# Performance work log

Hardware: AMD Instinct MI355X
Metric: run time of the kernel (lower is better)

The kernel has to match this reference:

```python
import jax, jax.numpy as jnp
import numpy as np

HIDDEN = 2048
NUM_HEADS = 16
HEAD_DIM = 128
INNER = NUM_HEADS * HEAD_DIM
ROPE_BASE = 10000.0


def apply_rope(x):
    # x: [B, H, S, D], rotate-half (NeoX-style) RoPE
    B, H, S, D = x.shape
    inv_freq = 1.0 / (ROPE_BASE ** (jnp.arange(0, D, 2, dtype=jnp.float32) / D))
    t = jnp.arange(S, dtype=jnp.float32)
    freqs = t[:, None] * inv_freq[None, :]          # [S, D/2]
    cos = jnp.concatenate([jnp.cos(freqs)] * 2, -1)  # [S, D]
    sin = jnp.concatenate([jnp.sin(freqs)] * 2, -1)
    x1, x2 = x[..., : D // 2], x[..., D // 2:]
    rotated = jnp.concatenate([-x2, x1], axis=-1)
    return x * cos[None, None] + rotated * sin[None, None]


def setup_inputs() -> dict:
    key = jax.random.key(0)
    ks = jax.random.split(key, 9)
    s = 1.0 / np.sqrt(HIDDEN)
    return {
        "hidden_states": jax.random.normal(ks[0], (2, 2048, HIDDEN), jnp.float32),
        "Wq": jax.random.uniform(ks[1], (INNER, HIDDEN), jnp.float32, -s, s),
        "bq": jax.random.uniform(ks[2], (INNER,), jnp.float32, -s, s),
        "Wk": jax.random.uniform(ks[3], (INNER, HIDDEN), jnp.float32, -s, s),
        "bk": jax.random.uniform(ks[4], (INNER,), jnp.float32, -s, s),
        "Wv": jax.random.uniform(ks[5], (INNER, HIDDEN), jnp.float32, -s, s),
        "bv": jax.random.uniform(ks[6], (INNER,), jnp.float32, -s, s),
        "Wo": jax.random.uniform(ks[7], (HIDDEN, INNER), jnp.float32, -s, s),
        "bo": jax.random.uniform(ks[8], (HIDDEN,), jnp.float32, -s, s),
    }


def reference(hidden_states, Wq, bq, Wk, bk, Wv, bv, Wo, bo):
    B, S, _ = hidden_states.shape

    def heads(x):  # [B,S,inner] -> [B,H,S,D]
        return x.reshape(B, S, NUM_HEADS, HEAD_DIM).transpose(0, 2, 1, 3)

    q = heads(hidden_states @ Wq.T + bq)
    k = heads(hidden_states @ Wk.T + bk)
    v = heads(hidden_states @ Wv.T + bv)
    q = apply_rope(q)
    k = apply_rope(k)

    scores = jnp.einsum("bhqd,bhkd->bhqk", q, k) / jnp.sqrt(
        jnp.asarray(HEAD_DIM, q.dtype))
    causal = jnp.tril(jnp.ones((S, S), dtype=bool))
    scores = jnp.where(causal[None, None], scores, jnp.finfo(scores.dtype).min)
    weights = jax.nn.softmax(scores, axis=-1)
    context = jnp.einsum("bhqk,bhkd->bhqd", weights, v)
    merged = context.transpose(0, 2, 1, 3).reshape(B, S, INNER)
    return merged @ Wo.T + bo
```

## Files before the change

### kernel.cpp

```cpp
#include <hip/hip_runtime.h>

using u16 = unsigned short;
using u32 = unsigned int;

typedef __attribute__((ext_vector_type(4))) float f32x4;
typedef __attribute__((ext_vector_type(8))) short frag8;

#define HIDDEN 2048
#define SEQ    2048
#define NHEADS 16
#define HDIM   128

__device__ __forceinline__ float bf2f(u16 u) {
  union { u32 i; float f; } c; c.i = ((u32)u) << 16; return c.f;
}
__device__ __forceinline__ u16 f2bf(float f) {
  union { float f; u32 i; } c; c.f = f;
  u32 u = c.i + 0x7fffu + ((c.i >> 16) & 1u);
  return (u16)(u >> 16);
}

__global__ void cvt_all(const float* __restrict__ X,
                        const float* __restrict__ W0, const float* __restrict__ W1,
                        const float* __restrict__ W2, const float* __restrict__ W3,
                        u16* __restrict__ dX,
                        u16* __restrict__ dW0, u16* __restrict__ dW1,
                        u16* __restrict__ dW2, u16* __restrict__ dW3)
{
  const int bx = blockIdx.x;
  const float* s; u16* d; int g;
  if (bx < 4096) { s = X; d = dX; g = bx * 256 + threadIdx.x; }
  else {
    const int t = bx - 4096;
    const int w = t >> 11;
    s = (w == 0) ? W0 : (w == 1) ? W1 : (w == 2) ? W2 : W3;
    d = (w == 0) ? dW0 : (w == 1) ? dW1 : (w == 2) ? dW2 : dW3;
    g = (t & 2047) * 256 + threadIdx.x;
  }
  const float* p = s + (size_t)g * 8;
  f32x4 x0 = *(const f32x4*)p, x1 = *(const f32x4*)(p + 4);
  frag8 o;
#pragma unroll
  for (int e = 0; e < 4; e++) { o[e] = (short)f2bf(x0[e]); o[e+4] = (short)f2bf(x1[e]); }
  *(frag8*)(d + (size_t)g * 8) = o;
}

template<int W_BF16, int NW, int VT, int C_F32>
__global__ __launch_bounds__(256, 4)
void gemm_fused(const u16* __restrict__ A,
                const void* __restrict__ W0, const void* __restrict__ W1,
                const void* __restrict__ W2,
                const float* __restrict__ bias0, const float* __restrict__ bias1,
                const float* __restrict__ bias2,
                void* __restrict__ C0, void* __restrict__ C1, void* __restrict__ C2)
{
  __shared__ __align__(16) u16 smem[8192];
  u16* As = smem;
  u16* Bs = smem + 4096;

  const int tid  = threadIdx.x;
  const int lane = tid & 63;
  const int wv   = tid >> 6;
  const int quad = lane >> 4;
  const int l16  = lane & 15;
  const int wm = wv >> 1, wn = wv & 1;
  const int m0 = blockIdx.y * 128;
  const int wix = (NW == 1) ? 0 : (blockIdx.x >> 4);
  const int n0  = ((NW == 1) ? blockIdx.x : (blockIdx.x & 15)) * 128;

  const void* Wp = (wix == 0) ? W0 : (wix == 1) ? W1 : W2;
  const float* bias = (wix == 0) ? bias0 : (wix == 1) ? bias1 : bias2;
  void* Cp = (wix == 0) ? C0 : (wix == 1) ? C1 : C2;

  f32x4 acc[4][4];
#pragma unroll
  for (int i = 0; i < 4; i++)
#pragma unroll
    for (int j = 0; j < 4; j++) acc[i][j] = (f32x4)0.0f;

  const int g0 = tid, g1 = tid + 256;
  const int r0 = g0 >> 2, c0 = (g0 & 3) * 8;
  const int r1 = g1 >> 2, c1 = (g1 & 3) * 8;

  for (int k0 = 0; k0 < HIDDEN; k0 += 32) {
    __builtin_amdgcn_global_load_lds(
      (const __attribute__((address_space(1))) void*)(A + (size_t)(m0 + r0) * HIDDEN + k0 + c0),
      (__attribute__((address_space(3))) void*)(As + g0 * 8), 16, 0, 0);
    __builtin_amdgcn_global_load_lds(
      (const __attribute__((address_space(1))) void*)(A + (size_t)(m0 + r1) * HIDDEN + k0 + c1),
      (__attribute__((address_space(3))) void*)(As + g1 * 8), 16, 0, 0);
    if (W_BF16) {
      const u16* Wb = (const u16*)Wp;
      __builtin_amdgcn_global_load_lds(
        (const __attribute__((address_space(1))) void*)(Wb + (size_t)(n0 + r0) * HIDDEN + k0 + c0),
        (__attribute__((address_space(3))) void*)(Bs + g0 * 8), 16, 0, 0);
      __builtin_amdgcn_global_load_lds(
        (const __attribute__((address_space(1))) void*)(Wb + (size_t)(n0 + r1) * HIDDEN + k0 + c1),
        (__attribute__((address_space(3))) void*)(Bs + g1 * 8), 16, 0, 0);
    } else {
      const float* Wf = (const float*)Wp;
      const float* p0 = Wf + (size_t)(n0 + r0) * HIDDEN + k0 + c0;
      const float* p1 = Wf + (size_t)(n0 + r1) * HIDDEN + k0 + c1;
      f32x4 x0 = *(const f32x4*)p0, x1 = *(const f32x4*)(p0 + 4);
      f32x4 y0 = *(const f32x4*)p1, y1 = *(const f32x4*)(p1 + 4);
      frag8 b0v, b1v;
#pragma unroll
      for (int e = 0; e < 4; e++) {
        b0v[e]   = (short)f2bf(x0[e]); b0v[e+4] = (short)f2bf(x1[e]);
        b1v[e]   = (short)f2bf(y0[e]); b1v[e+4] = (short)f2bf(y1[e]);
      }
      *(frag8*)&Bs[g0 * 8] = b0v;
      *(frag8*)&Bs[g1 * 8] = b1v;
    }

    __builtin_amdgcn_s_waitcnt(0);
    __syncthreads();

    frag8 af[4], bfr[4];
#pragma unroll
    for (int mt = 0; mt < 4; mt++)
      af[mt] = *(const frag8*)&As[(wm*64 + mt*16 + l16) * 32 + quad*8];
#pragma unroll
    for (int nt = 0; nt < 4; nt++)
      bfr[nt] = *(const frag8*)&Bs[(wn*64 + nt*16 + l16) * 32 + quad*8];
#pragma unroll
    for (int mt = 0; mt < 4; mt++)
#pragma unroll
      for (int nt = 0; nt < 4; nt++)
        acc[mt][nt] = __builtin_amdgcn_mfma_f32_16x16x32_bf16(af[mt], bfr[nt], acc[mt][nt], 0, 0, 0);

    __syncthreads();
  }

  if (VT && wix == 2) {
    u16* Cv = (u16*)Cp;
    u16* T = smem + wv * 1056;
#pragma unroll
    for (int nt = 0; nt < 4; nt++) {
      const int n  = n0 + wn*64 + nt*16 + l16;
      const float bv = bias[n];
#pragma unroll
      for (int mt = 0; mt < 4; mt++)
#pragma unroll
        for (int r = 0; r < 4; r++)
          T[l16 * 66 + mt*16 + quad*4 + r] = f2bf(acc[mt][nt][r] + bv);
#pragma unroll
      for (int rr = 0; rr < 16; rr++) {
        const int nn = n0 + wn*64 + nt*16 + rr;
        const int mm = m0 + wm*64 + lane;
        const int b = mm >> 11, s = mm & 2047;
        Cv[((size_t)(b * HIDDEN + nn)) * SEQ + s] = T[rr * 66 + lane];
      }
    }
  } else {
#pragma unroll
    for (int nt = 0; nt < 4; nt++) {
      const int n  = n0 + wn*64 + nt*16 + l16;
      const float bv = bias[n];
#pragma unroll
      for (int mt = 0; mt < 4; mt++) {
#pragma unroll
        for (int r = 0; r < 4; r++) {
          const int m = m0 + wm*64 + mt*16 + quad*4 + r;
          if (C_F32) ((float*)Cp)[(size_t)m * HIDDEN + n] = acc[mt][nt][r] + bv;
          else       ((u16*)Cp)[(size_t)m * HIDDEN + n]   = f2bf(acc[mt][nt][r] + bv);
        }
      }
    }
  }
}

#define NT32 32

#define STG(gptr, lofs) __builtin_amdgcn_global_load_lds( \
    (const __attribute__((address_space(1))) void*)(gptr), \
    (__attribute__((address_space(3))) void*)(smem + (lofs)), 16, 0, 0)

#define GRP(t, DOSTAGE, WAITSTR) { \
  u16* As = smem + ((t) % 3) * 24576; \
  u16* Bs = As + 16384; \
  frag8 af[8], bfr[2]; \
  _Pragma("unroll") for (int mt = 0; mt < 8; mt++) \
    af[mt] = *(const frag8*)(As + abase + mt*1024 + s0q); \
  bfr[0] = *(const frag8*)(Bs + bbase + s0q); \
  bfr[1] = *(const frag8*)(Bs + bbase + 1024 + s0q); \
  if (DOSTAGE) { \
    const size_t ko = (size_t)((t)+2)*64; const int sb = (((t)+2)%3)*24576; \
    STG(gA0 + ko, sb + ldsA0); STG(gA1 + ko, sb + ldsA1); STG(gB0 + ko, sb + ldsB0); \
  } \
  __builtin_amdgcn_s_barrier(); \
  __builtin_amdgcn_s_setprio(1); \
  _Pragma("unroll") for (int mt = 0; mt < 8; mt++) { \
    acc[mt][0] = __builtin_amdgcn_mfma_f32_16x16x32_bf16(af[mt], bfr[0], acc[mt][0], 0,0,0); \
    acc[mt][1] = __builtin_amdgcn_mfma_f32_16x16x32_bf16(af[mt], bfr[1], acc[mt][1], 0,0,0); \
  } \
  __builtin_amdgcn_s_setprio(0); \
  __builtin_amdgcn_s_barrier(); \
  _Pragma("unroll") for (int mt = 0; mt < 8; mt++) \
    af[mt] = *(const frag8*)(As + abase + mt*1024 + s1q); \
  bfr[0] = *(const frag8*)(Bs + bbase + s1q); \
  bfr[1] = *(const frag8*)(Bs + bbase + 1024 + s1q); \
  if (DOSTAGE) { \
    const size_t ko = (size_t)((t)+2)*64; const int sb = (((t)+2)%3)*24576; \
    STG(gA2 + ko, sb + ldsA2); STG(gA3 + ko, sb + ldsA3); STG(gB1 + ko, sb + ldsB1); \
  } \
  __builtin_amdgcn_s_barrier(); \
  __builtin_amdgcn_s_setprio(1); \
  _Pragma("unroll") for (int mt = 0; mt < 8; mt++) { \
    acc[mt][0] = __builtin_amdgcn_mfma_f32_16x16x32_bf16(af[mt], bfr[0], acc[mt][0], 0,0,0); \
    acc[mt][1] = __builtin_amdgcn_mfma_f32_16x16x32_bf16(af[mt], bfr[1], acc[mt][1], 0,0,0); \
  } \
  __builtin_amdgcn_s_setprio(0); \
  asm volatile("s_waitcnt " WAITSTR ::: "memory"); \
  __builtin_amdgcn_s_barrier(); \
}

#define G256_SETUP(Abase, Wbase) \
  const int tid  = threadIdx.x; \
  const int lane = tid & 63; \
  const int wv   = tid >> 6; \
  const int quad = lane >> 4; \
  const int l16  = lane & 15; \
  const int wm = wv >> 2, wn = wv & 3; \
  const int c8 = (lane & 7) ^ (lane >> 3); \
  const int rA = lane >> 3; \
  const u16* gA0 = (Abase) + (size_t)(m0 + wv*32 +  0 + rA) * HIDDEN + c8*8; \
  const u16* gA1 = (Abase) + (size_t)(m0 + wv*32 +  8 + rA) * HIDDEN + c8*8; \
  const u16* gA2 = (Abase) + (size_t)(m0 + wv*32 + 16 + rA) * HIDDEN + c8*8; \
  const u16* gA3 = (Abase) + (size_t)(m0 + wv*32 + 24 + rA) * HIDDEN + c8*8; \
  const u16* gB0 = (Wbase) + (size_t)(n0 + wv*16 +  0 + rA) * HIDDEN + c8*8; \
  const u16* gB1 = (Wbase) + (size_t)(n0 + wv*16 +  8 + rA) * HIDDEN + c8*8; \
  const int ldsA0 = (4*wv)*512 + lane*8; \
  const int ldsA1 = ldsA0 + 512; \
  const int ldsA2 = ldsA0 + 1024; \
  const int ldsA3 = ldsA0 + 1536; \
  const int ldsB0 = 16384 + (2*wv)*512 + lane*8; \
  const int ldsB1 = ldsB0 + 512; \
  const int s0q = ((quad    ) ^ (l16 & 7)) * 8; \
  const int s1q = ((quad + 4) ^ (l16 & 7)) * 8; \
  const int abase = (wm*128 + l16) * 64; \
  const int bbase = (wn*32  + l16) * 64; \
  f32x4 acc[8][2]; \
  _Pragma("unroll") \
  for (int i = 0; i < 8; i++) { acc[i][0] = (f32x4)0.0f; acc[i][1] = (f32x4)0.0f; } \
  STG(gA0, ldsA0); STG(gA1, ldsA1); STG(gB0, ldsB0); \
  STG(gA2, ldsA2); STG(gA3, ldsA3); STG(gB1, ldsB1); \
  STG(gA0 + 64, 24576 + ldsA0); STG(gA1 + 64, 24576 + ldsA1); STG(gB0 + 64, 24576 + ldsB0); \
  STG(gA2 + 64, 24576 + ldsA2); STG(gA3 + 64, 24576 + ldsA3); STG(gB1 + 64, 24576 + ldsB1); \
  asm volatile("s_waitcnt vmcnt(6)" ::: "memory"); \
  __builtin_amdgcn_s_barrier(); \
  for (int t = 0; t < NT32 - 2; ++t) GRP(t, 1, "vmcnt(6)"); \
  GRP(NT32 - 2, 0, "vmcnt(0)"); \
  GRP(NT32 - 1, 0, "vmcnt(63)");

__global__ __launch_bounds__(512, 2)
void gemm256_qkv(const u16* __restrict__ A,
                 const u16* __restrict__ W0, const u16* __restrict__ W1,
                 const u16* __restrict__ W2,
                 const float* __restrict__ bias0, const float* __restrict__ bias1,
                 const float* __restrict__ bias2,
                 u16* __restrict__ C0, u16* __restrict__ C1, u16* __restrict__ Vt)
{
  __shared__ __align__(16) u16 smem[73728];

  const int bid = blockIdx.x;
  const int sbid = (bid & 7) * 96 + (bid >> 3);
  const int colTile = sbid >> 4;
  const int rowTile = sbid & 15;
  const int wix = colTile >> 4;
  const int n0  = (colTile & 15) * 128;
  const int m0  = rowTile * 256;

  const u16* Wp = (wix == 0) ? W0 : (wix == 1) ? W1 : W2;
  const float* bias = (wix == 0) ? bias0 : (wix == 1) ? bias1 : bias2;

  G256_SETUP(A, Wp)

  if (wix != 2) {
    u16* Cb = (wix == 0) ? C0 : C1;
#pragma unroll
    for (int nt = 0; nt < 2; nt++) {
      const int n = n0 + wn*32 + nt*16 + l16;
      const float bv = bias[n];
#pragma unroll
      for (int mt = 0; mt < 8; mt++) {
        const int m = m0 + wm*128 + mt*16 + quad*4;
#pragma unroll
        for (int r = 0; r < 4; r++)
          Cb[(size_t)(m + r) * HIDDEN + n] = f2bf(acc[mt][nt][r] + bv);
      }
    }
  } else {
    u16* T = smem + wv * 2176;
    const int b  = m0 >> 11;
    const int s0 = (m0 & 2047) + wm*128;
#pragma unroll
    for (int nt = 0; nt < 2; nt++) {
      const int nloc = n0 + wn*32 + nt*16;
      const float bv = bias[nloc + l16];
#pragma unroll
      for (int mt = 0; mt < 8; mt++)
#pragma unroll
        for (int r = 0; r < 4; r++)
          T[l16*136 + mt*16 + quad*4 + r] = f2bf(acc[mt][nt][r] + bv);
#pragma unroll
      for (int rr = 0; rr < 16; rr++) {
        const size_t vb = ((size_t)(b * HIDDEN + nloc + rr)) * SEQ + s0;
        Vt[vb + lane]      = T[rr*136 + lane];
        Vt[vb + 64 + lane] = T[rr*136 + 64 + lane];
      }
    }
  }
}

__global__ __launch_bounds__(512, 2)
void gemm256_o(const u16* __restrict__ A, const u16* __restrict__ W,
               const float* __restrict__ bias, float* __restrict__ C)
{
  __shared__ __align__(16) u16 smem[73728];

  const int bid = blockIdx.x;
  const int sbid = (bid & 7) * 32 + (bid >> 3);
  const int colTile = sbid >> 4;
  const int rowTile = sbid & 15;
  const int n0  = colTile * 128;
  const int m0  = rowTile * 256;

  G256_SETUP(A, W)

#pragma unroll
  for (int nt = 0; nt < 2; nt++) {
    const int n = n0 + wn*32 + nt*16 + l16;
    const float bv = bias[n];
#pragma unroll
    for (int mt = 0; mt < 8; mt++) {
      const int m = m0 + wm*128 + mt*16 + quad*4;
#pragma unroll
      for (int r = 0; r < 4; r++)
        C[(size_t)(m + r) * HIDDEN + n] = acc[mt][nt][r] + bv;
    }
  }
}

__global__ void rope_kernel(u16* __restrict__ Q, u16* __restrict__ K)
{
  const int tid = blockIdx.x * 256 + threadIdx.x;
  const int t   = tid >> 19;
  const int r   = tid & 524287;
  const int row = r >> 7;
  const int grp = r & 127;
  const int h   = grp >> 3, d0 = (grp & 7) * 8;
  u16* X = t ? K : Q;
  const float s = (float)(row & 2047);
  const float qscale = t ? 1.0f : 0.08838834764831845f;
  const size_t base = (size_t)row * HIDDEN + h * HDIM + d0;
  frag8 a = *(const frag8*)(X + base);
  frag8 b = *(const frag8*)(X + base + 64);
  frag8 oa, ob;
#pragma unroll
  for (int e = 0; e < 8; e++) {
    const float inv = __expf(-(float)(d0 + e) * (9.210340371976184f / 64.0f));
    float sn, c;
    __sincosf(s * inv, &sn, &c);
    const float x1 = bf2f((u16)a[e]), x2 = bf2f((u16)b[e]);
    oa[e] = (short)f2bf((x1 * c - x2 * sn) * qscale);
    ob[e] = (short)f2bf((x2 * c + x1 * sn) * qscale);
  }
  *(frag8*)(X + base)      = oa;
  *(frag8*)(X + base + 64) = ob;
}

#define KS_STR 132
#define VS_STR 68
#define PS_STR 68
__global__ __launch_bounds__(256, 3)
void attn_kernel(const u16* Q, const u16* __restrict__ K,
                 const u16* __restrict__ Vt, u16* O)
{
  __shared__ __align__(16) u16 Ks[64 * KS_STR];
  __shared__ __align__(16) u16 Vs[128 * VS_STR];
  __shared__ __align__(16) u16 Ps[4 * 16 * PS_STR];

  const int bx = blockIdx.x;
  const int g  = bx >> 5;
  const int bh = bx & 31;
  const int qt = (g & 1) ? (31 - (g >> 1)) : (g >> 1);
  const int b = bh >> 4, h = bh & 15;

  const int tid = threadIdx.x, lane = tid & 63, wv = tid >> 6;
  const int quad = lane >> 4, l16 = lane & 15;

  frag8 qf[4];
  const size_t qbase = ((size_t)(b * SEQ) + qt*64 + wv*16) * HIDDEN + h * HDIM;
#pragma unroll
  for (int ks = 0; ks < 4; ks++)
    qf[ks] = *(const frag8*)(Q + qbase + (size_t)l16 * HIDDEN + ks*32 + quad*8);

  f32x4 Oacc[8];
#pragma unroll
  for (int dt = 0; dt < 8; dt++) Oacc[dt] = (f32x4)0.0f;
  float m_i[4], l_i[4];
#pragma unroll
  for (int r = 0; r < 4; r++) { m_i[r] = -1e30f; l_i[r] = 0.0f; }

  const int ktmax = qt + 1;
  const size_t krow0 = (size_t)(b * SEQ) * HIDDEN + h * HDIM;
  const size_t vrow0 = (size_t)(b * HIDDEN + h * HDIM) * SEQ;
  u16* Pw = Ps + wv * (16 * PS_STR);
  const int qmin = qt*64 + wv*16;

  const int kkey = tid >> 4, kgd = (tid & 15) * 8;
  const int vd = tid >> 3, vj8 = (tid & 7) * 8;

  frag8 kreg[4], vreg[4];
#pragma unroll
  for (int it = 0; it < 4; it++) {
    kreg[it] = *(const frag8*)(K + krow0 + (size_t)(it*16 + kkey) * HIDDEN + kgd);
    vreg[it] = *(const frag8*)(Vt + vrow0 + (size_t)(it*32 + vd) * SEQ + vj8);
  }

  for (int kt = 0; kt < ktmax; kt++) {
#pragma unroll
    for (int it = 0; it < 4; it++) {
      *(frag8*)&Ks[(it*16 + kkey) * KS_STR + kgd] = kreg[it];
      *(frag8*)&Vs[(it*32 + vd) * VS_STR + vj8]  = vreg[it];
    }
    __syncthreads();

    if (kt + 1 < ktmax) {
#pragma unroll
      for (int it = 0; it < 4; it++) {
        kreg[it] = *(const frag8*)(K + krow0 + (size_t)((kt+1)*64 + it*16 + kkey) * HIDDEN + kgd);
        vreg[it] = *(const frag8*)(Vt + vrow0 + (size_t)(it*32 + vd) * SEQ + (kt+1)*64 + vj8);
      }
    }

    f32x4 st[4];
#pragma unroll
    for (int jt = 0; jt < 4; jt++) st[jt] = (f32x4)0.0f;

    __builtin_amdgcn_s_setprio(1);
#pragma unroll
    for (int ks = 0; ks < 4; ks++) {
      frag8 kf[4];
#pragma unroll
      for (int jt = 0; jt < 4; jt++)
        kf[jt] = *(const frag8*)&Ks[(jt*16 + l16) * KS_STR + ks*32 + quad*8];
#pragma unroll
      for (int jt = 0; jt < 4; jt++)
        st[jt] = __builtin_amdgcn_mfma_f32_16x16x32_bf16(qf[ks], kf[jt], st[jt], 0, 0, 0);
    }
    __builtin_amdgcn_s_setprio(0);

    if (kt == qt) {
#pragma unroll
      for (int jt = 0; jt < 4; jt++) {
        const int jl = jt*16 + l16;
#pragma unroll
        for (int r = 0; r < 4; r++) {
          const int ml = wv*16 + quad*4 + r;
          st[jt][r] = (jl <= ml) ? st[jt][r] : -1e30f;
        }
      }
    }

    float alpha[4];
    int needresc = 0;
#pragma unroll
    for (int r = 0; r < 4; r++) {
      float cm = st[0][r];
#pragma unroll
      for (int jt = 1; jt < 4; jt++) cm = fmaxf(cm, st[jt][r]);
      cm = fmaxf(cm, __shfl_xor(cm, 1, 64));
      cm = fmaxf(cm, __shfl_xor(cm, 2, 64));
      cm = fmaxf(cm, __shfl_xor(cm, 4, 64));
      cm = fmaxf(cm, __shfl_xor(cm, 8, 64));
      if (cm > m_i[r] + 8.0f) {
        alpha[r] = __expf(m_i[r] - cm);
        m_i[r] = cm;
        needresc = 1;
      } else {
        alpha[r] = 1.0f;
      }
    }

    float csum[4];
#pragma unroll
    for (int r = 0; r < 4; r++) csum[r] = 0.0f;
#pragma unroll
    for (int jt = 0; jt < 4; jt++)
#pragma unroll
      for (int r = 0; r < 4; r++) {
        const float p = __expf(st[jt][r] - m_i[r]);
        csum[r] += p;
        Pw[(quad*4 + r) * PS_STR + jt*16 + l16] = f2bf(p);
      }
#pragma unroll
    for (int r = 0; r < 4; r++) {
      float cs = csum[r];
      cs += __shfl_xor(cs, 1, 64);
      cs += __shfl_xor(cs, 2, 64);
      cs += __shfl_xor(cs, 4, 64);
      cs += __shfl_xor(cs, 8, 64);
      l_i[r] = l_i[r] * alpha[r] + cs;
    }
    if (__any(needresc)) {
#pragma unroll
      for (int r = 0; r < 4; r++)
#pragma unroll
        for (int dt = 0; dt < 8; dt++) Oacc[dt][r] *= alpha[r];
    }

    __builtin_amdgcn_s_setprio(1);
#pragma unroll
    for (int ks2 = 0; ks2 < 2; ks2++) {
      frag8 pf = *(const frag8*)&Pw[l16 * PS_STR + ks2*32 + quad*8];
#pragma unroll
      for (int dt = 0; dt < 8; dt++) {
        frag8 vf = *(const frag8*)&Vs[(dt*16 + l16) * VS_STR + ks2*32 + quad*8];
        Oacc[dt] = __builtin_amdgcn_mfma_f32_16x16x32_bf16(pf, vf, Oacc[dt], 0, 0, 0);
      }
    }
    __builtin_amdgcn_s_setprio(0);
    __syncthreads();
  }

#pragma unroll
  for (int r = 0; r < 4; r++) {
    const float inv = 1.0f / l_i[r];
    const int m = qmin + quad*4 + r;
#pragma unroll
    for (int dt = 0; dt < 8; dt++) {
      const int d = dt*16 + l16;
      O[((size_t)(b * SEQ) + m) * HIDDEN + h * HDIM + d] = f2bf(Oacc[dt][r] * inv);
    }
  }
}

extern "C" void kernel_launch(void* const* d_in, const int* in_sizes, int n_in,
                              void* d_out, int out_size, void* d_ws, size_t ws_size,
                              hipStream_t stream)
{
  const float* X  = (const float*)d_in[0];
  const float* Wq = (const float*)d_in[1];
  const float* bq = (const float*)d_in[2];
  const float* Wk = (const float*)d_in[3];
  const float* bk = (const float*)d_in[4];
  const float* Wv = (const float*)d_in[5];
  const float* bv = (const float*)d_in[6];
  const float* Wo = (const float*)d_in[7];
  const float* bo = (const float*)d_in[8];
  float* out = (float*)d_out;

  u16* Kb = (u16*)d_out;
  u16* Xb = (u16*)d_out + (8u << 20);
  char* ws = (char*)d_ws;
  u16* Qb  = (u16*)ws;
  u16* Vtb = (u16*)(ws + (16u << 20));

  dim3 blk(256);
  const bool fast = ws_size >= (64u << 20);
  if (fast) {
    u16* Wqb = (u16*)(ws + (32u << 20));
    u16* Wkb = (u16*)(ws + (40u << 20));
    u16* Wvb = (u16*)(ws + (48u << 20));
    u16* Wob = (u16*)(ws + (56u << 20));
    cvt_all<<<12288, blk, 0, stream>>>(X, Wq, Wk, Wv, Wo, Xb, Wqb, Wkb, Wvb, Wob);
    gemm256_qkv<<<dim3(768), dim3(512), 0, stream>>>(
        Xb, Wqb, Wkb, Wvb, bq, bk, bv, Qb, Kb, Vtb);
    rope_kernel<<<4096, blk, 0, stream>>>(Qb, Kb);
    attn_kernel<<<1024, blk, 0, stream>>>(Qb, Kb, Vtb, Qb);
    gemm256_o<<<dim3(256), dim3(512), 0, stream>>>(Qb, Wob, bo, out);
  } else {
    cvt_all<<<4096, blk, 0, stream>>>(X, Wq, Wk, Wv, Wo, Xb, Xb, Xb, Xb, Xb);
    gemm_fused<0,3,1,0><<<dim3(48,32), blk, 0, stream>>>(
        Xb, Wq, Wk, Wv, bq, bk, bv, Qb, Kb, Vtb);
    rope_kernel<<<4096, blk, 0, stream>>>(Qb, Kb);
    attn_kernel<<<1024, blk, 0, stream>>>(Qb, Kb, Vtb, Qb);
    gemm_fused<0,1,0,1><<<dim3(16,32), blk, 0, stream>>>(
        Qb, Wo, Wo, Wo, bo, bo, bo, out, out, out);
  }
}
```

Measured before the change: 429.5 us.

## Enlarge attention query tile to 128 rows with direct global-to-LDS swizzled loads

Each attention block now handles 128 query rows (two 16-row fragments per wave), so every K/V tile loaded into shared memory feeds twice as many MFMAs, and the grid shrinks from 1024 to 512 blocks. K/V tiles are loaded with global_load_lds straight into XOR-swizzled shared memory instead of through registers, which removes the padded layouts. The register prefetch of the next tile is dropped, so each iteration waits for vmcnt(0) before computing and load latency is no longer overlapped. Register use roughly doubles, and occupancy is lowered to 2 blocks per SIMD.

Measured after the change: 430.3 us. Within noise of the previous version (+0.2%).

```diff
diff --git a/kernel.cpp b/kernel.cpp
--- a/kernel.cpp
+++ b/kernel.cpp
@@ -370,74 +370,80 @@
   *(frag8*)(X + base + 64) = ob;
 }
 
-#define KS_STR 132
-#define VS_STR 68
 #define PS_STR 68
-__global__ __launch_bounds__(256, 3)
+__global__ __launch_bounds__(256, 2)
 void attn_kernel(const u16* Q, const u16* __restrict__ K,
                  const u16* __restrict__ Vt, u16* O)
 {
-  __shared__ __align__(16) u16 Ks[64 * KS_STR];
-  __shared__ __align__(16) u16 Vs[128 * VS_STR];
-  __shared__ __align__(16) u16 Ps[4 * 16 * PS_STR];
+  __shared__ __align__(16) u16 smem[25088];
 
   const int bx = blockIdx.x;
   const int g  = bx >> 5;
   const int bh = bx & 31;
-  const int qt = (g & 1) ? (31 - (g >> 1)) : (g >> 1);
+  const int qt = (g & 1) ? (15 - (g >> 1)) : (g >> 1);
   const int b = bh >> 4, h = bh & 15;
 
   const int tid = threadIdx.x, lane = tid & 63, wv = tid >> 6;
   const int quad = lane >> 4, l16 = lane & 15;
-
-  frag8 qf[4];
-  const size_t qbase = ((size_t)(b * SEQ) + qt*64 + wv*16) * HIDDEN + h * HDIM;
-#pragma unroll
-  for (int ks = 0; ks < 4; ks++)
-    qf[ks] = *(const frag8*)(Q + qbase + (size_t)l16 * HIDDEN + ks*32 + quad*8);
-
-  f32x4 Oacc[8];
-#pragma unroll
-  for (int dt = 0; dt < 8; dt++) Oacc[dt] = (f32x4)0.0f;
-  float m_i[4], l_i[4];
-#pragma unroll
-  for (int r = 0; r < 4; r++) { m_i[r] = -1e30f; l_i[r] = 0.0f; }
-
-  const int ktmax = qt + 1;
+  const int l7 = l16 & 7;
+
   const size_t krow0 = (size_t)(b * SEQ) * HIDDEN + h * HDIM;
   const size_t vrow0 = (size_t)(b * HIDDEN + h * HDIM) * SEQ;
-  u16* Pw = Ps + wv * (16 * PS_STR);
-  const int qmin = qt*64 + wv*16;
-
-  const int kkey = tid >> 4, kgd = (tid & 15) * 8;
-  const int vd = tid >> 3, vj8 = (tid & 7) * 8;
-
-  frag8 kreg[4], vreg[4];
+
+  frag8 qf[2][4];
+  const size_t qbase = ((size_t)(b * SEQ) + qt*128 + wv*32) * HIDDEN + h * HDIM;
+#pragma unroll
+  for (int mq = 0; mq < 2; mq++)
+#pragma unroll
+    for (int ks = 0; ks < 4; ks++)
+      qf[mq][ks] = *(const frag8*)(Q + qbase + (size_t)(mq*16 + l16) * HIDDEN + ks*32 + quad*8);
+
+  const int kr4 = lane >> 4, kc = lane & 15;
+  const int vr8 = lane >> 3;
+  const u16* gK[4]; const u16* gV[4];
+  int ldsK[4], ldsV[4];
 #pragma unroll
   for (int it = 0; it < 4; it++) {
-    kreg[it] = *(const frag8*)(K + krow0 + (size_t)(it*16 + kkey) * HIDDEN + kgd);
-    vreg[it] = *(const frag8*)(Vt + vrow0 + (size_t)(it*32 + vd) * SEQ + vj8);
-  }
+    const int kcs = kc ^ ((it*4 + kr4) & 7);
+    gK[it] = K + krow0 + (size_t)(wv*16 + it*4 + kr4) * HIDDEN + kcs*8;
+    ldsK[it] = (wv*16 + it*4)*128 + lane*8;
+    const int vcs = (lane & 7) ^ vr8;
+    gV[it] = Vt + vrow0 + (size_t)(wv*32 + it*8 + vr8) * SEQ + vcs*8;
+    ldsV[it] = 8192 + (wv*32 + it*8)*64 + lane*8;
+  }
+
+  f32x4 Oacc[2][8];
+#pragma unroll
+  for (int mq = 0; mq < 2; mq++)
+#pragma unroll
+    for (int dt = 0; dt < 8; dt++) Oacc[mq][dt] = (f32x4)0.0f;
+  float m_i[2][4], l_i[2][4];
+#pragma unroll
+  for (int mq = 0; mq < 2; mq++)
+#pragma unroll
+    for (int r = 0; r < 4; r++) { m_i[mq][r] = -1e30f; l_i[mq][r] = 0.0f; }
+
+  const int ktmax = 2*qt + 2;
+  u16* Pp = smem + 16384 + wv*2176;
 
   for (int kt = 0; kt < ktmax; kt++) {
 #pragma unroll
     for (int it = 0; it < 4; it++) {
-      *(frag8*)&Ks[(it*16 + kkey) * KS_STR + kgd] = kreg[it];
-      *(frag8*)&Vs[(it*32 + vd) * VS_STR + vj8]  = vreg[it];
-    }
+      __builtin_amdgcn_global_load_lds(
+        (const __attribute__((address_space(1))) void*)(gK[it] + (size_t)kt*64*HIDDEN),
+        (__attribute__((address_space(3))) void*)(smem + ldsK[it]), 16, 0, 0);
+      __builtin_amdgcn_global_load_lds(
+        (const __attribute__((address_space(1))) void*)(gV[it] + kt*64),
+        (__attribute__((address_space(3))) void*)(smem + ldsV[it]), 16, 0, 0);
+    }
+    asm volatile("s_waitcnt vmcnt(0)" ::: "memory");
     __syncthreads();
 
-    if (kt + 1 < ktmax) {
-#pragma unroll
-      for (int it = 0; it < 4; it++) {
-        kreg[it] = *(const frag8*)(K + krow0 + (size_t)((kt+1)*64 + it*16 + kkey) * HIDDEN + kgd);
-        vreg[it] = *(const frag8*)(Vt + vrow0 + (size_t)(it*32 + vd) * SEQ + (kt+1)*64 + vj8);
-      }
-    }
-
-    f32x4 st[4];
-#pragma unroll
-    for (int jt = 0; jt < 4; jt++) st[jt] = (f32x4)0.0f;
+    f32x4 st[2][4];
+#pragma unroll
+    for (int mq = 0; mq < 2; mq++)
+#pragma unroll
+      for (int jt = 0; jt < 4; jt++) st[mq][jt] = (f32x4)0.0f;
 
     __builtin_amdgcn_s_setprio(1);
 #pragma unroll
@@ -445,80 +451,92 @@
       frag8 kf[4];
 #pragma unroll
       for (int jt = 0; jt < 4; jt++)
-        kf[jt] = *(const frag8*)&Ks[(jt*16 + l16) * KS_STR + ks*32 + quad*8];
+        kf[jt] = *(const frag8*)&smem[(jt*16 + l16)*128 + (((ks*4+quad) ^ l7))*8];
+#pragma unroll
+      for (int jt = 0; jt < 4; jt++) {
+        st[0][jt] = __builtin_amdgcn_mfma_f32_16x16x32_bf16(qf[0][ks], kf[jt], st[0][jt], 0, 0, 0);
+        st[1][jt] = __builtin_amdgcn_mfma_f32_16x16x32_bf16(qf[1][ks], kf[jt], st[1][jt], 0, 0, 0);
+      }
+    }
+    __builtin_amdgcn_s_setprio(0);
+
+    if (kt >= 2*qt) {
+#pragma unroll
+      for (int mq = 0; mq < 2; mq++)
+#pragma unroll
+        for (int jt = 0; jt < 4; jt++) {
+          const int jl = kt*64 + jt*16 + l16;
+#pragma unroll
+          for (int r = 0; r < 4; r++) {
+            const int ml = qt*128 + wv*32 + mq*16 + quad*4 + r;
+            st[mq][jt][r] = (jl <= ml) ? st[mq][jt][r] : -1e30f;
+          }
+        }
+    }
+
+    float alpha[2][4];
+    int needresc = 0;
+#pragma unroll
+    for (int mq = 0; mq < 2; mq++)
+#pragma unroll
+      for (int r = 0; r < 4; r++) {
+        float cm = fmaxf(fmaxf(st[mq][0][r], st[mq][1][r]),
+                         fmaxf(st[mq][2][r], st[mq][3][r]));
+        cm = fmaxf(cm, __shfl_xor(cm, 1, 64));
+        cm = fmaxf(cm, __shfl_xor(cm, 2, 64));
+        cm = fmaxf(cm, __shfl_xor(cm, 4, 64));
+        cm = fmaxf(cm, __shfl_xor(cm, 8, 64));
+        if (cm > m_i[mq][r] + 8.0f) {
+          alpha[mq][r] = __expf(m_i[mq][r] - cm);
+          m_i[mq][r] = cm;
+          needresc = 1;
+        } else {
+          alpha[mq][r] = 1.0f;
+        }
+      }
+
+#pragma unroll
+    for (int mq = 0; mq < 2; mq++) {
+      float csum[4];
+#pragma unroll
+      for (int r = 0; r < 4; r++) csum[r] = 0.0f;
 #pragma unroll
       for (int jt = 0; jt < 4; jt++)
-        st[jt] = __builtin_amdgcn_mfma_f32_16x16x32_bf16(qf[ks], kf[jt], st[jt], 0, 0, 0);
-    }
-    __builtin_amdgcn_s_setprio(0);
-
-    if (kt == qt) {
-#pragma unroll
-      for (int jt = 0; jt < 4; jt++) {
-        const int jl = jt*16 + l16;
 #pragma unroll
         for (int r = 0; r < 4; r++) {
-          const int ml = wv*16 + quad*4 + r;
-          st[jt][r] = (jl <= ml) ? st[jt][r] : -1e30f;
+          const float p = __expf(st[mq][jt][r] - m_i[mq][r]);
+          csum[r] += p;
+          Pp[mq*1088 + (quad*4 + r) * PS_STR + jt*16 + l16] = f2bf(p);
         }
-      }
-    }
-
-    float alpha[4];
-    int needresc = 0;
-#pragma unroll
-    for (int r = 0; r < 4; r++) {
-      float cm = st[0][r];
-#pragma unroll
-      for (int jt = 1; jt < 4; jt++) cm = fmaxf(cm, st[jt][r]);
-      cm = fmaxf(cm, __shfl_xor(cm, 1, 64));
-      cm = fmaxf(cm, __shfl_xor(cm, 2, 64));
-      cm = fmaxf(cm, __shfl_xor(cm, 4, 64));
-      cm = fmaxf(cm, __shfl_xor(cm, 8, 64));
-      if (cm > m_i[r] + 8.0f) {
-        alpha[r] = __expf(m_i[r] - cm);
-        m_i[r] = cm;
-        needresc = 1;
-      } else {
-        alpha[r] = 1.0f;
-      }
-    }
-
-    float csum[4];
-#pragma unroll
-    for (int r = 0; r < 4; r++) csum[r] = 0.0f;
-#pragma unroll
-    for (int jt = 0; jt < 4; jt++)
 #pragma unroll
       for (int r = 0; r < 4; r++) {
-        const float p = __expf(st[jt][r] - m_i[r]);
-        csum[r] += p;
-        Pw[(quad*4 + r) * PS_STR + jt*16 + l16] = f2bf(p);
-      }
-#pragma unroll
-    for (int r = 0; r < 4; r++) {
-      float cs = csum[r];
-      cs += __shfl_xor(cs, 1, 64);
-      cs += __shfl_xor(cs, 2, 64);
-      cs += __shfl_xor(cs, 4, 64);
-      cs += __shfl_xor(cs, 8, 64);
-      l_i[r] = l_i[r] * alpha[r] + cs;
+        float cs = csum[r];
+        cs += __shfl_xor(cs, 1, 64);
+        cs += __shfl_xor(cs, 2, 64);
+        cs += __shfl_xor(cs, 4, 64);
+        cs += __shfl_xor(cs, 8, 64);
+        l_i[mq][r] = l_i[mq][r] * alpha[mq][r] + cs;
+      }
     }
     if (__any(needresc)) {
 #pragma unroll
-      for (int r = 0; r < 4; r++)
-#pragma unroll
-        for (int dt = 0; dt < 8; dt++) Oacc[dt][r] *= alpha[r];
+      for (int mq = 0; mq < 2; mq++)
+#pragma unroll
+        for (int r = 0; r < 4; r++)
+#pragma unroll
+          for (int dt = 0; dt < 8; dt++) Oacc[mq][dt][r] *= alpha[mq][r];
     }
 
     __builtin_amdgcn_s_setprio(1);
 #pragma unroll
     for (int ks2 = 0; ks2 < 2; ks2++) {
-      frag8 pf = *(const frag8*)&Pw[l16 * PS_STR + ks2*32 + quad*8];
+      frag8 pf0 = *(const frag8*)&Pp[l16 * PS_STR + ks2*32 + quad*8];
+      frag8 pf1 = *(const frag8*)&Pp[1088 + l16 * PS_STR + ks2*32 + quad*8];
 #pragma unroll
       for (int dt = 0; dt < 8; dt++) {
-        frag8 vf = *(const frag8*)&Vs[(dt*16 + l16) * VS_STR + ks2*32 + quad*8];
-        Oacc[dt] = __builtin_amdgcn_mfma_f32_16x16x32_bf16(pf, vf, Oacc[dt], 0, 0, 0);
+        frag8 vf = *(const frag8*)&smem[8192 + (dt*16 + l16)*64 + ((ks2*4+quad) ^ l7)*8];
+        Oacc[0][dt] = __builtin_amdgcn_mfma_f32_16x16x32_bf16(pf0, vf, Oacc[0][dt], 0, 0, 0);
+        Oacc[1][dt] = __builtin_amdgcn_mfma_f32_16x16x32_bf16(pf1, vf, Oacc[1][dt], 0, 0, 0);
       }
     }
     __builtin_amdgcn_s_setprio(0);
@@ -526,15 +544,17 @@
   }
 
 #pragma unroll
-  for (int r = 0; r < 4; r++) {
-    const float inv = 1.0f / l_i[r];
-    const int m = qmin + quad*4 + r;
-#pragma unroll
-    for (int dt = 0; dt < 8; dt++) {
-      const int d = dt*16 + l16;
-      O[((size_t)(b * SEQ) + m) * HIDDEN + h * HDIM + d] = f2bf(Oacc[dt][r] * inv);
-    }
-  }
+  for (int mq = 0; mq < 2; mq++)
+#pragma unroll
+    for (int r = 0; r < 4; r++) {
+      const float inv = 1.0f / l_i[mq][r];
+      const int m = qt*128 + wv*32 + mq*16 + quad*4 + r;
+#pragma unroll
+      for (int dt = 0; dt < 8; dt++) {
+        const int d = dt*16 + l16;
+        O[((size_t)(b * SEQ) + m) * HIDDEN + h * HDIM + d] = f2bf(Oacc[mq][dt][r] * inv);
+      }
+    }
 }
 
 extern "C" void kernel_launch(void* const* d_in, const int* in_sizes, int n_in,
@@ -569,14 +589,14 @@
     gemm256_qkv<<<dim3(768), dim3(512), 0, stream>>>(
         Xb, Wqb, Wkb, Wvb, bq, bk, bv, Qb, Kb, Vtb);
     rope_kernel<<<4096, blk, 0, stream>>>(Qb, Kb);
-    attn_kernel<<<1024, blk, 0, stream>>>(Qb, Kb, Vtb, Qb);
+    attn_kernel<<<512, blk, 0, stream>>>(Qb, Kb, Vtb, Qb);
     gemm256_o<<<dim3(256), dim3(512), 0, stream>>>(Qb, Wob, bo, out);
   } else {
     cvt_all<<<4096, blk, 0, stream>>>(X, Wq, Wk, Wv, Wo, Xb, Xb, Xb, Xb, Xb);
     gemm_fused<0,3,1,0><<<dim3(48,32), blk, 0, stream>>>(
         Xb, Wq, Wk, Wv, bq, bk, bv, Qb, Kb, Vtb);
     rope_kernel<<<4096, blk, 0, stream>>>(Qb, Kb);
-    attn_kernel<<<1024, blk, 0, stream>>>(Qb, Kb, Vtb, Qb);
+    attn_kernel<<<512, blk, 0, stream>>>(Qb, Kb, Vtb, Qb);
     gemm_fused<0,1,0,1><<<dim3(16,32), blk, 0, stream>>>(
         Qb, Wo, Wo, Wo, bo, bo, bo, out, out, out);
   }
```

## Load K/V tiles directly into LDS with XOR-swizzled layout in attention

Applied to the files above, without the earlier changes.

Replaces the register-staged K/V prefetch with direct global-to-LDS loads (global_load_lds), stores K, V and P tiles unpadded with an XOR swizzle to avoid bank conflicts, and raises the occupancy hint from 3 to 4 blocks per CU. This cuts register pressure and the VGPR-to-LDS copy, and shrinks LDS use so more blocks can fit. The cost is losing the software prefetch: every iteration now waits for vmcnt(0) before compute, so load latency is no longer overlapped except through other resident waves.

Result: slower. 444.3 us (+3.4%).

```diff
diff --git a/kernel.cpp b/kernel.cpp
--- a/kernel.cpp
+++ b/kernel.cpp
@@ -370,16 +370,11 @@
   *(frag8*)(X + base + 64) = ob;
 }
 
-#define KS_STR 132
-#define VS_STR 68
-#define PS_STR 68
-__global__ __launch_bounds__(256, 3)
+__global__ __launch_bounds__(256, 4)
 void attn_kernel(const u16* Q, const u16* __restrict__ K,
                  const u16* __restrict__ Vt, u16* O)
 {
-  __shared__ __align__(16) u16 Ks[64 * KS_STR];
-  __shared__ __align__(16) u16 Vs[128 * VS_STR];
-  __shared__ __align__(16) u16 Ps[4 * 16 * PS_STR];
+  __shared__ __align__(16) u16 smem[20480];
 
   const int bx = blockIdx.x;
   const int g  = bx >> 5;
@@ -389,6 +384,10 @@
 
   const int tid = threadIdx.x, lane = tid & 63, wv = tid >> 6;
   const int quad = lane >> 4, l16 = lane & 15;
+  const int l7 = l16 & 7;
+
+  const size_t krow0 = (size_t)(b * SEQ) * HIDDEN + h * HDIM;
+  const size_t vrow0 = (size_t)(b * HIDDEN + h * HDIM) * SEQ;
 
   frag8 qf[4];
   const size_t qbase = ((size_t)(b * SEQ) + qt*64 + wv*16) * HIDDEN + h * HDIM;
@@ -396,6 +395,20 @@
   for (int ks = 0; ks < 4; ks++)
     qf[ks] = *(const frag8*)(Q + qbase + (size_t)l16 * HIDDEN + ks*32 + quad*8);
 
+  const int kr4 = lane >> 4, kc = lane & 15;
+  const int vr8 = lane >> 3;
+  const u16* gK[4]; const u16* gV[4];
+  int ldsK[4], ldsV[4];
+#pragma unroll
+  for (int it = 0; it < 4; it++) {
+    const int kcs = kc ^ ((it*4 + kr4) & 7);
+    gK[it] = K + krow0 + (size_t)(wv*16 + it*4 + kr4) * HIDDEN + kcs*8;
+    ldsK[it] = (wv*16 + it*4)*128 + lane*8;
+    const int vcs = (lane & 7) ^ vr8;
+    gV[it] = Vt + vrow0 + (size_t)(wv*32 + it*8 + vr8) * SEQ + vcs*8;
+    ldsV[it] = 8192 + (wv*32 + it*8)*64 + lane*8;
+  }
+
   f32x4 Oacc[8];
 #pragma unroll
   for (int dt = 0; dt < 8; dt++) Oacc[dt] = (f32x4)0.0f;
@@ -404,36 +417,20 @@
   for (int r = 0; r < 4; r++) { m_i[r] = -1e30f; l_i[r] = 0.0f; }
 
   const int ktmax = qt + 1;
-  const size_t krow0 = (size_t)(b * SEQ) * HIDDEN + h * HDIM;
-  const size_t vrow0 = (size_t)(b * HIDDEN + h * HDIM) * SEQ;
-  u16* Pw = Ps + wv * (16 * PS_STR);
-  const int qmin = qt*64 + wv*16;
-
-  const int kkey = tid >> 4, kgd = (tid & 15) * 8;
-  const int vd = tid >> 3, vj8 = (tid & 7) * 8;
-
-  frag8 kreg[4], vreg[4];
-#pragma unroll
-  for (int it = 0; it < 4; it++) {
-    kreg[it] = *(const frag8*)(K + krow0 + (size_t)(it*16 + kkey) * HIDDEN + kgd);
-    vreg[it] = *(const frag8*)(Vt + vrow0 + (size_t)(it*32 + vd) * SEQ + vj8);
-  }
+  u16* Pw = smem + 16384 + wv*1024;
 
   for (int kt = 0; kt < ktmax; kt++) {
 #pragma unroll
     for (int it = 0; it < 4; it++) {
-      *(frag8*)&Ks[(it*16 + kkey) * KS_STR + kgd] = kreg[it];
-      *(frag8*)&Vs[(it*32 + vd) * VS_STR + vj8]  = vreg[it];
-    }
+      __builtin_amdgcn_global_load_lds(
+        (const __attribute__((address_space(1))) void*)(gK[it] + (size_t)kt*64*HIDDEN),
+        (__attribute__((address_space(3))) void*)(smem + ldsK[it]), 16, 0, 0);
+      __builtin_amdgcn_global_load_lds(
+        (const __attribute__((address_space(1))) void*)(gV[it] + kt*64),
+        (__attribute__((address_space(3))) void*)(smem + ldsV[it]), 16, 0, 0);
+    }
+    asm volatile("s_waitcnt vmcnt(0)" ::: "memory");
     __syncthreads();
-
-    if (kt + 1 < ktmax) {
-#pragma unroll
-      for (int it = 0; it < 4; it++) {
-        kreg[it] = *(const frag8*)(K + krow0 + (size_t)((kt+1)*64 + it*16 + kkey) * HIDDEN + kgd);
-        vreg[it] = *(const frag8*)(Vt + vrow0 + (size_t)(it*32 + vd) * SEQ + (kt+1)*64 + vj8);
-      }
-    }
 
     f32x4 st[4];
 #pragma unroll
@@ -445,7 +442,7 @@
       frag8 kf[4];
 #pragma unroll
       for (int jt = 0; jt < 4; jt++)
-        kf[jt] = *(const frag8*)&Ks[(jt*16 + l16) * KS_STR + ks*32 + quad*8];
+        kf[jt] = *(const frag8*)&smem[(jt*16 + l16)*128 + ((ks*4 + quad) ^ l7)*8];
 #pragma unroll
       for (int jt = 0; jt < 4; jt++)
         st[jt] = __builtin_amdgcn_mfma_f32_16x16x32_bf16(qf[ks], kf[jt], st[jt], 0, 0, 0);
@@ -468,9 +465,7 @@
     int needresc = 0;
 #pragma unroll
     for (int r = 0; r < 4; r++) {
-      float cm = st[0][r];
-#pragma unroll
-      for (int jt = 1; jt < 4; jt++) cm = fmaxf(cm, st[jt][r]);
+      float cm = fmaxf(fmaxf(st[0][r], st[1][r]), fmaxf(st[2][r], st[3][r]));
       cm = fmaxf(cm, __shfl_xor(cm, 1, 64));
       cm = fmaxf(cm, __shfl_xor(cm, 2, 64));
       cm = fmaxf(cm, __shfl_xor(cm, 4, 64));
@@ -493,7 +488,8 @@
       for (int r = 0; r < 4; r++) {
         const float p = __expf(st[jt][r] - m_i[r]);
         csum[r] += p;
-        Pw[(quad*4 + r) * PS_STR + jt*16 + l16] = f2bf(p);
+        const int prow = quad*4 + r;
+        Pw[prow*64 + (((jt*2 + (l16 >> 3)) ^ (prow & 7)) << 3) + l7] = f2bf(p);
       }
 #pragma unroll
     for (int r = 0; r < 4; r++) {
@@ -514,10 +510,10 @@
     __builtin_amdgcn_s_setprio(1);
 #pragma unroll
     for (int ks2 = 0; ks2 < 2; ks2++) {
-      frag8 pf = *(const frag8*)&Pw[l16 * PS_STR + ks2*32 + quad*8];
+      frag8 pf = *(const frag8*)&Pw[l16*64 + ((ks2*4 + quad) ^ l7)*8];
 #pragma unroll
       for (int dt = 0; dt < 8; dt++) {
-        frag8 vf = *(const frag8*)&Vs[(dt*16 + l16) * VS_STR + ks2*32 + quad*8];
+        frag8 vf = *(const frag8*)&smem[8192 + (dt*16 + l16)*64 + ((ks2*4 + quad) ^ l7)*8];
         Oacc[dt] = __builtin_amdgcn_mfma_f32_16x16x32_bf16(pf, vf, Oacc[dt], 0, 0, 0);
       }
     }
@@ -528,7 +524,7 @@
 #pragma unroll
   for (int r = 0; r < 4; r++) {
     const float inv = 1.0f / l_i[r];
-    const int m = qmin + quad*4 + r;
+    const int m = qt*64 + wv*16 + quad*4 + r;
 #pragma unroll
     for (int dt = 0; dt < 8; dt++) {
       const int d = dt*16 + l16;
```

## Fuse RoPE and Q scaling into QKV GEMM epilogue; simplify attention loop

Applied to the files above, without the earlier changes.

Applies rotary embeddings and the 1/sqrt(head_dim) scaling on Q inside the QKV GEMM epilogue. Each tile is staged through shared memory so one thread can pair the two halves of a head. This removes the separate rope kernel launch and its extra read and write of Q and K. The attention kernel also drops its register prefetch of the next K/V tile, the s_setprio hints and the thresholded lazy rescale, so it now loads K/V straight into LDS and always rescales. That simplification may lose load/compute overlap in attention, and the sincos work now lands in the GEMM epilogue.

After: 430.2 us. About the same (+0.2%).

```diff
diff --git a/kernel.cpp b/kernel.cpp
--- a/kernel.cpp
+++ b/kernel.cpp
@@ -277,18 +277,42 @@
   G256_SETUP(A, Wp)
 
   if (wix != 2) {
+    const float scale = (wix == 0) ? 0.08838834764831845f : 1.0f;
+    u16* T = smem;
+#pragma unroll
+    for (int nt = 0; nt < 2; nt++) {
+      const int nl = wn*32 + nt*16 + l16;
+      const float bv = bias[n0 + nl];
+#pragma unroll
+      for (int mt = 0; mt < 8; mt++) {
+        const int ml = wm*128 + mt*16 + quad*4;
+#pragma unroll
+        for (int r = 0; r < 4; r++)
+          T[(ml + r)*128 + nl] = f2bf((acc[mt][nt][r] + bv) * scale);
+      }
+    }
+    __syncthreads();
+
     u16* Cb = (wix == 0) ? C0 : C1;
-#pragma unroll
-    for (int nt = 0; nt < 2; nt++) {
-      const int n = n0 + wn*32 + nt*16 + l16;
-      const float bv = bias[n];
-#pragma unroll
-      for (int mt = 0; mt < 8; mt++) {
-        const int m = m0 + wm*128 + mt*16 + quad*4;
-#pragma unroll
-        for (int r = 0; r < 4; r++)
-          Cb[(size_t)(m + r) * HIDDEN + n] = f2bf(acc[mt][nt][r] + bv);
-      }
+    const int mr = tid >> 1, qd = tid & 1;
+    const float s = (float)((m0 + mr) & 2047);
+#pragma unroll
+    for (int c8i = 0; c8i < 4; c8i++) {
+      const int d0 = qd*32 + c8i*8;
+      frag8 lo = *(const frag8*)&T[mr*128 + d0];
+      frag8 hi = *(const frag8*)&T[mr*128 + 64 + d0];
+      frag8 olo, ohi;
+#pragma unroll
+      for (int e = 0; e < 8; e++) {
+        const float inv = __expf(-(float)(d0 + e) * (9.210340371976184f / 64.0f));
+        float sn, c;
+        __sincosf(s * inv, &sn, &c);
+        const float x1 = bf2f((u16)lo[e]), x2 = bf2f((u16)hi[e]);
+        olo[e] = (short)f2bf(x1 * c - x2 * sn);
+        ohi[e] = (short)f2bf(x2 * c + x1 * sn);
+      }
+      *(frag8*)&Cb[(size_t)(m0 + mr) * HIDDEN + n0 + d0]      = olo;
+      *(frag8*)&Cb[(size_t)(m0 + mr) * HIDDEN + n0 + 64 + d0] = ohi;
     }
   } else {
     u16* T = smem + wv * 2176;
@@ -409,37 +433,27 @@
   u16* Pw = Ps + wv * (16 * PS_STR);
   const int qmin = qt*64 + wv*16;
 
-  const int kkey = tid >> 4, kgd = (tid & 15) * 8;
-  const int vd = tid >> 3, vj8 = (tid & 7) * 8;
-
-  frag8 kreg[4], vreg[4];
-#pragma unroll
-  for (int it = 0; it < 4; it++) {
-    kreg[it] = *(const frag8*)(K + krow0 + (size_t)(it*16 + kkey) * HIDDEN + kgd);
-    vreg[it] = *(const frag8*)(Vt + vrow0 + (size_t)(it*32 + vd) * SEQ + vj8);
-  }
-
   for (int kt = 0; kt < ktmax; kt++) {
 #pragma unroll
     for (int it = 0; it < 4; it++) {
-      *(frag8*)&Ks[(it*16 + kkey) * KS_STR + kgd] = kreg[it];
-      *(frag8*)&Vs[(it*32 + vd) * VS_STR + vj8]  = vreg[it];
+      const int G = it * 256 + tid;
+      const int key = G >> 4, gd = (G & 15) * 8;
+      *(frag8*)&Ks[key * KS_STR + gd] =
+        *(const frag8*)(K + krow0 + (size_t)(kt*64 + key) * HIDDEN + gd);
+    }
+#pragma unroll
+    for (int it = 0; it < 4; it++) {
+      const int G = it * 256 + tid;
+      const int d = G >> 3, j8 = (G & 7) * 8;
+      *(frag8*)&Vs[d * VS_STR + j8] =
+        *(const frag8*)(Vt + vrow0 + (size_t)d * SEQ + kt*64 + j8);
     }
     __syncthreads();
 
-    if (kt + 1 < ktmax) {
-#pragma unroll
-      for (int it = 0; it < 4; it++) {
-        kreg[it] = *(const frag8*)(K + krow0 + (size_t)((kt+1)*64 + it*16 + kkey) * HIDDEN + kgd);
-        vreg[it] = *(const frag8*)(Vt + vrow0 + (size_t)(it*32 + vd) * SEQ + (kt+1)*64 + vj8);
-      }
-    }
-
     f32x4 st[4];
 #pragma unroll
     for (int jt = 0; jt < 4; jt++) st[jt] = (f32x4)0.0f;
 
-    __builtin_amdgcn_s_setprio(1);
 #pragma unroll
     for (int ks = 0; ks < 4; ks++) {
       frag8 kf[4];
@@ -450,7 +464,6 @@
       for (int jt = 0; jt < 4; jt++)
         st[jt] = __builtin_amdgcn_mfma_f32_16x16x32_bf16(qf[ks], kf[jt], st[jt], 0, 0, 0);
     }
-    __builtin_amdgcn_s_setprio(0);
 
     if (kt == qt) {
 #pragma unroll
@@ -465,7 +478,6 @@
     }
 
     float alpha[4];
-    int needresc = 0;
 #pragma unroll
     for (int r = 0; r < 4; r++) {
       float cm = st[0][r];
@@ -475,13 +487,9 @@
       cm = fmaxf(cm, __shfl_xor(cm, 2, 64));
       cm = fmaxf(cm, __shfl_xor(cm, 4, 64));
       cm = fmaxf(cm, __shfl_xor(cm, 8, 64));
-      if (cm > m_i[r] + 8.0f) {
-        alpha[r] = __expf(m_i[r] - cm);
-        m_i[r] = cm;
-        needresc = 1;
-      } else {
-        alpha[r] = 1.0f;
-      }
+      const float mnew = fmaxf(m_i[r], cm);
+      alpha[r] = __expf(m_i[r] - mnew);
+      m_i[r] = mnew;
     }
 
     float csum[4];
@@ -503,15 +511,10 @@
       cs += __shfl_xor(cs, 4, 64);
       cs += __shfl_xor(cs, 8, 64);
       l_i[r] = l_i[r] * alpha[r] + cs;
-    }
-    if (__any(needresc)) {
-#pragma unroll
-      for (int r = 0; r < 4; r++)
-#pragma unroll
-        for (int dt = 0; dt < 8; dt++) Oacc[dt][r] *= alpha[r];
-    }
-
-    __builtin_amdgcn_s_setprio(1);
+#pragma unroll
+      for (int dt = 0; dt < 8; dt++) Oacc[dt][r] *= alpha[r];
+    }
+
 #pragma unroll
     for (int ks2 = 0; ks2 < 2; ks2++) {
       frag8 pf = *(const frag8*)&Pw[l16 * PS_STR + ks2*32 + quad*8];
@@ -521,7 +524,6 @@
         Oacc[dt] = __builtin_amdgcn_mfma_f32_16x16x32_bf16(pf, vf, Oacc[dt], 0, 0, 0);
       }
     }
-    __builtin_amdgcn_s_setprio(0);
     __syncthreads();
   }
 
@@ -568,7 +570,6 @@
     cvt_all<<<12288, blk, 0, stream>>>(X, Wq, Wk, Wv, Wo, Xb, Wqb, Wkb, Wvb, Wob);
     gemm256_qkv<<<dim3(768), dim3(512), 0, stream>>>(
         Xb, Wqb, Wkb, Wvb, bq, bk, bv, Qb, Kb, Vtb);
-    rope_kernel<<<4096, blk, 0, stream>>>(Qb, Kb);
     attn_kernel<<<1024, blk, 0, stream>>>(Qb, Kb, Vtb, Qb);
     gemm256_o<<<dim3(256), dim3(512), 0, stream>>>(Qb, Wob, bo, out);
   } else {
```
